# Kernel tuning notes

Hardware: AMD Instinct MI355X
Metric: run time of the kernel (lower is better)

Reference implementation:

```python
import jax, jax.numpy as jnp
import numpy as np

GROUPS = 32
EPS = 1e-6


def group_norm(x, gamma, beta):
    b, h, w, c = x.shape
    xg = x.reshape(b, h, w, GROUPS, c // GROUPS)
    mean = jnp.mean(xg, axis=(1, 2, 4), keepdims=True)
    var = jnp.var(xg, axis=(1, 2, 4), keepdims=True)
    xg = (xg - mean) * jax.lax.rsqrt(var + EPS)
    return xg.reshape(b, h, w, c) * gamma + beta


def setup_inputs() -> dict:
    key = jax.random.key(0)
    ks = jax.random.split(key, 6)
    B, H, W, C = 4, 64, 64, 512
    scale = 0.02
    return {
        "x": jax.random.normal(ks[0], (B, H, W, C), dtype=jnp.float32),
        "gamma": jnp.ones((C,), dtype=jnp.float32),
        "beta": jnp.zeros((C,), dtype=jnp.float32),
        "wq": jax.random.normal(ks[1], (C, C), dtype=jnp.float32) * scale,
        "bq": jnp.zeros((C,), dtype=jnp.float32),
        "wk": jax.random.normal(ks[2], (C, C), dtype=jnp.float32) * scale,
        "bk": jnp.zeros((C,), dtype=jnp.float32),
        "wv": jax.random.normal(ks[3], (C, C), dtype=jnp.float32) * scale,
        "bv": jnp.zeros((C,), dtype=jnp.float32),
        "wo": jax.random.normal(ks[4], (C, C), dtype=jnp.float32) * scale,
        "bo": jnp.zeros((C,), dtype=jnp.float32),
    }


def reference(x, gamma, beta, wq, bq, wk, bk, wv, bv, wo, bo):
    b, h, w, c = x.shape
    xn = group_norm(x, gamma, beta)
    # 1x1 convs == per-pixel linear layers
    q = (jnp.einsum('bhwc,cd->bhwd', xn, wq) + bq).reshape(b, h * w, c)
    k = (jnp.einsum('bhwc,cd->bhwd', xn, wk) + bk).reshape(b, h * w, c)
    v = (jnp.einsum('bhwc,cd->bhwd', xn, wv) + bv).reshape(b, h * w, c)
    # full (hw x hw) attention, single head
    scores = jnp.einsum('bic,bjc->bij', q, k) * (c ** -0.5)  # [b, hw, hw]
    attn = jax.nn.softmax(scores, axis=-1)
    out = jnp.einsum('bij,bjc->bic', attn, v).reshape(b, h, w, c)
    return jnp.einsum('bhwc,cd->bhwd', out, wo) + bo + x
```

## Files before the change

### kernel.cpp

```cpp
#include <hip/hip_runtime.h>
#include <stdint.h>


typedef __attribute__((ext_vector_type(8))) short bf16x8;
typedef __attribute__((ext_vector_type(8))) unsigned short u16x8;
typedef __attribute__((ext_vector_type(4))) float f32x4;

#define SOFTMAX_SCALE 0.044194173824159216f

__device__ __forceinline__ unsigned short f2bf(float f) {
  unsigned int x = __float_as_uint(f);
  x += 0x7fffu + ((x >> 16) & 1u);
  return (unsigned short)(x >> 16);
}
__device__ __forceinline__ float bf2f(unsigned short u) {
  return __uint_as_float((unsigned int)u << 16);
}

__device__ __forceinline__ void gl_lds16(const void* g, void* l) {
  __builtin_amdgcn_global_load_lds(
      (__attribute__((address_space(1))) unsigned char*)g,
      (__attribute__((address_space(3))) unsigned char*)l, 16, 0, 0);
}

__device__ __forceinline__ void gemm_tile(
    const unsigned short* __restrict__ A, long lda,
    const unsigned short* __restrict__ B, long ldb,
    int K, unsigned short* As, unsigned short* Bs, f32x4 acc[4][4]) {
  const int tid = threadIdx.x;
  const int wave = tid >> 6, lane = tid & 63;
  const int srow = lane >> 3;
  const int soff = ((lane & 7) ^ srow) * 16;
  const int wm = (wave >> 1) * 64, wn = (wave & 1) * 64;
  const int lrow = lane & 15;
  const int rsw = lrow & 7;
  const int kgb = lane >> 4;

  for (int k0 = 0; k0 < K; k0 += 64) {
    __syncthreads();
    for (int i = 0; i < 4; ++i) {
      int chunk = wave * 4 + i;
      int row = chunk * 8 + srow;
      gl_lds16((const char*)(A + (long)row * lda + k0) + soff, (char*)As + chunk * 1024);
      gl_lds16((const char*)(B + (long)row * ldb + k0) + soff, (char*)Bs + chunk * 1024);
    }
    __syncthreads();
#pragma unroll
    for (int ks = 0; ks < 2; ++ks) {
      bf16x8 af[4], bfr[4];
      const int off = ((ks * 4 + kgb) ^ rsw) * 8;
#pragma unroll
      for (int t = 0; t < 4; ++t) {
        af[t]  = *(const bf16x8*)&As[(wm + t * 16 + lrow) * 64 + off];
        bfr[t] = *(const bf16x8*)&Bs[(wn + t * 16 + lrow) * 64 + off];
      }
#pragma unroll
      for (int mt = 0; mt < 4; ++mt)
#pragma unroll
        for (int nt = 0; nt < 4; ++nt)
          acc[mt][nt] = __builtin_amdgcn_mfma_f32_16x16x32_bf16(af[mt], bfr[nt], acc[mt][nt], 0, 0, 0);
    }
  }
}

#define EPILOG_SETUP                                          \
  const int lane = threadIdx.x & 63, wave = threadIdx.x >> 6; \
  const int wm = (wave >> 1) * 64, wn = (wave & 1) * 64;      \
  const int lcol = lane & 15, lrb = (lane >> 4) * 4;

__global__ void prep_kernel(const float* __restrict__ wq, const float* __restrict__ wk,
                            const float* __restrict__ wv, const float* __restrict__ wo,
                            const float* __restrict__ bq, const float* __restrict__ bk,
                            const float* __restrict__ bv,
                            unsigned short* __restrict__ wqkvT,
                            unsigned short* __restrict__ woT,
                            float* __restrict__ bias, float* __restrict__ stats,
                            float* __restrict__ lsum) {
  long id = (long)blockIdx.x * 256 + threadIdx.x;
  if (id < 786432) {
    long n = id >> 9, k = id & 511;
    const float* w = (n < 512) ? wq : (n < 1024 ? wk : wv);
    wqkvT[id] = f2bf(w[k * 512 + (n & 511)]);
  } else if (id < 786432 + 262144) {
    long j = id - 786432, n = j >> 9, k = j & 511;
    woT[j] = f2bf(wo[k * 512 + n]);
  } else if (id < 786432 + 262144 + 1536) {
    long j = id - 786432 - 262144;
    bias[j] = (j < 512) ? bq[j] : (j < 1024 ? bk[j - 512] : bv[j - 1024]);
  } else if (id < 786432 + 262144 + 1536 + 256) {
    stats[id - 786432 - 262144 - 1536] = 0.f;
  } else if (id < 786432 + 262144 + 1536 + 256 + 16384) {
    lsum[id - 786432 - 262144 - 1536 - 256] = 0.f;
  }
}

__global__ __launch_bounds__(256) void gn_stats(const float* __restrict__ x,
                                                float* __restrict__ stats) {
  const int b = blockIdx.x >> 7, slab = blockIdx.x & 127;
  const float* xp = x + (long)b * 4096 * 512 + (long)slab * 32 * 512;
  const int tid = threadIdx.x;
  float s = 0.f, s2 = 0.f;
  for (int it = 0; it < 16; ++it) {
    int i = it * 256 + tid;
    float4 v = *(const float4*)(xp + (long)i * 4);
    s += v.x + v.y + v.z + v.w;
    s2 += v.x * v.x + v.y * v.y + v.z * v.z + v.w * v.w;
  }
  s += __shfl_xor(s, 1); s += __shfl_xor(s, 2);
  s2 += __shfl_xor(s2, 1); s2 += __shfl_xor(s2, 2);
  if ((tid & 3) == 0) {
    int g = (tid & 127) >> 2;
    atomicAdd(&stats[(b * 32 + g) * 2], s);
    atomicAdd(&stats[(b * 32 + g) * 2 + 1], s2);
  }
}

__global__ __launch_bounds__(256) void gn_apply(const float* __restrict__ x,
                                                const float* __restrict__ stats,
                                                const float* __restrict__ gamma,
                                                const float* __restrict__ beta,
                                                unsigned short* __restrict__ xn) {
  long id = (long)blockIdx.x * 256 + threadIdx.x;
  long a = id * 4;
  int b = (int)(id >> 19);
  int ch = (int)(a & 511);
  int g = ch >> 4;
  float s = stats[(b * 32 + g) * 2], s2 = stats[(b * 32 + g) * 2 + 1];
  float mean = s * (1.f / 65536.f);
  float rinv = rsqrtf(s2 * (1.f / 65536.f) - mean * mean + 1e-6f);
  float4 v = *(const float4*)(x + a);
  float4 gm = *(const float4*)(gamma + ch);
  float4 bt = *(const float4*)(beta + ch);
  ushort4 o;
  o.x = f2bf((v.x - mean) * rinv * gm.x + bt.x);
  o.y = f2bf((v.y - mean) * rinv * gm.y + bt.y);
  o.z = f2bf((v.z - mean) * rinv * gm.z + bt.z);
  o.w = f2bf((v.w - mean) * rinv * gm.w + bt.w);
  *(ushort4*)(xn + a) = o;
}

__global__ __launch_bounds__(256) void qkv_kernel(
    const unsigned short* __restrict__ xn, const unsigned short* __restrict__ wqkvT,
    const float* __restrict__ bias, unsigned short* __restrict__ q,
    unsigned short* __restrict__ kk, unsigned short* __restrict__ vv) {
  __shared__ unsigned short As[128 * 64], Bs[128 * 64];
  f32x4 acc[4][4] = {};
  const long tm = (long)blockIdx.x * 128, tn = (long)blockIdx.y * 128;
  gemm_tile(xn + tm * 512, 512, wqkvT + tn * 512, 512, 512, As, Bs, acc);
  EPILOG_SETUP
#pragma unroll
  for (int mt = 0; mt < 4; ++mt)
#pragma unroll
    for (int nt = 0; nt < 4; ++nt)
#pragma unroll
      for (int r = 0; r < 4; ++r) {
        long m = tm + wm + mt * 16 + lrb + r;
        long n = tn + wn + nt * 16 + lcol;
        float v = acc[mt][nt][r] + bias[n];
        if (n < 512)       q[m * 512 + n] = f2bf(v * SOFTMAX_SCALE);
        else if (n < 1024) kk[m * 512 + (n - 512)] = f2bf(v);
        else               vv[m * 512 + (n - 1024)] = f2bf(v);
      }
}

__global__ __launch_bounds__(256) void transpose_v(const unsigned short* __restrict__ v,
                                                   unsigned short* __restrict__ vT) {
  const int b = blockIdx.z;
  const long j0 = (long)blockIdx.x * 64, c0 = (long)blockIdx.y * 64;
  __shared__ unsigned short t[64][72];
  const int tc = (threadIdx.x & 15) * 4, tr = threadIdx.x >> 4;
  for (int rr = 0; rr < 64; rr += 16) {
    ushort4 u = *(const ushort4*)&v[((long)b * 4096 + j0 + tr + rr) * 512 + c0 + tc];
    t[tr + rr][tc] = u.x; t[tr + rr][tc + 1] = u.y;
    t[tr + rr][tc + 2] = u.z; t[tr + rr][tc + 3] = u.w;
  }
  __syncthreads();
  for (int rr = 0; rr < 64; rr += 16) {
    int c = tr + rr;
    ushort4 o;
    o.x = t[tc + 0][c]; o.y = t[tc + 1][c]; o.z = t[tc + 2][c]; o.w = t[tc + 3][c];
    *(ushort4*)&vT[((long)b * 512 + c0 + c) * 4096 + j0 + tc] = o;
  }
}

__global__ __launch_bounds__(256) void qkt_kernel(
    const unsigned short* __restrict__ q, const unsigned short* __restrict__ kk,
    unsigned short* __restrict__ probs, float* __restrict__ lsum, int b0) {
  __shared__ unsigned short As[128 * 64], Bs[128 * 64];
  f32x4 acc[4][4] = {};
  const int z = blockIdx.z;
  const long bb = (long)(b0 + z) * 4096 * 512;
  const long tm = (long)blockIdx.x * 128, tn = (long)blockIdx.y * 128;
  gemm_tile(q + bb + tm * 512, 512, kk + bb + tn * 512, 512, 512, As, Bs, acc);
  EPILOG_SETUP
  unsigned short* out = probs + (long)z * 4096 * 4096;
  float* ls = lsum + (long)(b0 + z) * 4096;
#pragma unroll
  for (int mt = 0; mt < 4; ++mt) {
    float rsum[4] = {0.f, 0.f, 0.f, 0.f};
#pragma unroll
    for (int nt = 0; nt < 4; ++nt)
#pragma unroll
      for (int r = 0; r < 4; ++r) {
        long m = tm + wm + mt * 16 + lrb + r;
        long n = tn + wn + nt * 16 + lcol;
        float e = __expf(acc[mt][nt][r]);
        unsigned short h = f2bf(e);
        out[m * 4096 + n] = h;
        rsum[r] += bf2f(h);
      }
#pragma unroll
    for (int r = 0; r < 4; ++r) {
      float s = rsum[r];
      s += __shfl_xor(s, 1); s += __shfl_xor(s, 2);
      s += __shfl_xor(s, 4); s += __shfl_xor(s, 8);
      if (lcol == 0) atomicAdd(&ls[tm + wm + mt * 16 + lrb + r], s);
    }
  }
}

__global__ __launch_bounds__(256) void pv_kernel(
    const unsigned short* __restrict__ probs, const unsigned short* __restrict__ vT,
    unsigned short* __restrict__ part, int b0) {
  __shared__ unsigned short As[128 * 64], Bs[128 * 64];
  f32x4 acc[4][4] = {};
  const int zb = blockIdx.z >> 2, s = blockIdx.z & 3;
  const long tm = (long)blockIdx.x * 128, tn = (long)blockIdx.y * 128;
  gemm_tile(probs + (long)zb * 4096 * 4096 + tm * 4096 + s * 1024, 4096,
            vT + (long)(b0 + zb) * 512 * 4096 + tn * 4096 + s * 1024, 4096,
            1024, As, Bs, acc);
  EPILOG_SETUP
  unsigned short* out = part + (long)blockIdx.z * 4096 * 512;
#pragma unroll
  for (int mt = 0; mt < 4; ++mt)
#pragma unroll
    for (int nt = 0; nt < 4; ++nt)
#pragma unroll
      for (int r = 0; r < 4; ++r) {
        long m = tm + wm + mt * 16 + lrb + r;
        long n = tn + wn + nt * 16 + lcol;
        out[m * 512 + n] = f2bf(acc[mt][nt][r]);
      }
}

__global__ __launch_bounds__(256) void reduce_kernel(const unsigned short* __restrict__ part,
                                                     const float* __restrict__ lsum,
                                                     unsigned short* __restrict__ attn,
                                                     int b0) {
  const long elems = 4096l * 512;
  const int zb = blockIdx.y;
  const unsigned short* pp = part + (long)zb * 4 * elems;
  long id = (long)blockIdx.x * 256 + threadIdx.x;
  long a = id * 8;
  int m = (int)(a >> 9);
  float inv = 1.f / lsum[(long)(b0 + zb) * 4096 + m];
  u16x8 p0 = *(const u16x8*)(pp + a);
  u16x8 p1 = *(const u16x8*)(pp + elems + a);
  u16x8 p2 = *(const u16x8*)(pp + 2 * elems + a);
  u16x8 p3 = *(const u16x8*)(pp + 3 * elems + a);
  u16x8 o;
#pragma unroll
  for (int j = 0; j < 8; ++j)
    o[j] = f2bf((bf2f(p0[j]) + bf2f(p1[j]) + bf2f(p2[j]) + bf2f(p3[j])) * inv);
  *(u16x8*)(attn + (long)(b0 + zb) * elems + a) = o;
}

__global__ __launch_bounds__(256) void proj_kernel(
    const unsigned short* __restrict__ attn, const unsigned short* __restrict__ woT,
    const float* __restrict__ bo, const float* __restrict__ x,
    float* __restrict__ out) {
  __shared__ unsigned short As[128 * 64], Bs[128 * 64];
  f32x4 acc[4][4] = {};
  const long tm = (long)blockIdx.x * 128, tn = (long)blockIdx.y * 128;
  gemm_tile(attn + tm * 512, 512, woT + tn * 512, 512, 512, As, Bs, acc);
  EPILOG_SETUP
#pragma unroll
  for (int mt = 0; mt < 4; ++mt)
#pragma unroll
    for (int nt = 0; nt < 4; ++nt)
#pragma unroll
      for (int r = 0; r < 4; ++r) {
        long m = tm + wm + mt * 16 + lrb + r;
        long n = tn + wn + nt * 16 + lcol;
        out[m * 512 + n] = acc[mt][nt][r] + bo[n] + x[m * 512 + n];
      }
}

extern "C" void kernel_launch(void* const* d_in, const int* in_sizes, int n_in,
                              void* d_out, int out_size, void* d_ws, size_t ws_size,
                              hipStream_t stream) {
  const float* x     = (const float*)d_in[0];
  const float* gamma = (const float*)d_in[1];
  const float* beta  = (const float*)d_in[2];
  const float* wq    = (const float*)d_in[3];
  const float* bq    = (const float*)d_in[4];
  const float* wk    = (const float*)d_in[5];
  const float* bk    = (const float*)d_in[6];
  const float* wv    = (const float*)d_in[7];
  const float* bv    = (const float*)d_in[8];
  const float* wo    = (const float*)d_in[9];
  const float* bo    = (const float*)d_in[10];

  char* p = (char*)d_ws;
  auto take = [&](size_t bytes) { char* r = p; p += (bytes + 255) & ~(size_t)255; return r; };
  const long NTOK = 16384, C = 512, HW = 4096;
  unsigned short* xn    = (unsigned short*)take(NTOK * C * 2);
  unsigned short* q     = (unsigned short*)take(NTOK * C * 2);
  unsigned short* kbuf  = (unsigned short*)take(NTOK * C * 2);
  unsigned short* vT    = (unsigned short*)take(NTOK * C * 2);
  unsigned short* wqkvT = (unsigned short*)take(1536l * 512 * 2);
  unsigned short* woT   = (unsigned short*)take(512l * 512 * 2);
  float* bias           = (float*)take(1536 * 4);
  float* stats          = (float*)take(256 * 4);
  float* lsum           = (float*)take(16384 * 4);

  size_t fixed = (size_t)(p - (char*)d_ws);
  size_t per_nb = (size_t)HW * HW * 2 + 4ul * HW * C * 2 + 512;
  int NB = (ws_size >= fixed + 4 * per_nb) ? 4
         : (ws_size >= fixed + 2 * per_nb) ? 2 : 1;
  unsigned short* probs = (unsigned short*)take((size_t)NB * HW * HW * 2);
  unsigned short* part  = (unsigned short*)take((size_t)NB * 4 * HW * C * 2);
  unsigned short* attn  = xn;
  unsigned short* vbuf  = part;

  prep_kernel<<<4168, 256, 0, stream>>>(wq, wk, wv, wo, bq, bk, bv, wqkvT, woT,
                                        bias, stats, lsum);
  gn_stats<<<512, 256, 0, stream>>>(x, stats);
  gn_apply<<<8192, 256, 0, stream>>>(x, stats, gamma, beta, xn);

  qkv_kernel<<<dim3(128, 12), 256, 0, stream>>>(xn, wqkvT, bias, q, kbuf, vbuf);
  transpose_v<<<dim3(64, 8, 4), 256, 0, stream>>>(vbuf, vT);

  for (int b0 = 0; b0 < 4; b0 += NB) {
    qkt_kernel<<<dim3(32, 32, NB), 256, 0, stream>>>(q, kbuf, probs, lsum, b0);
    pv_kernel<<<dim3(32, 4, 4 * NB), 256, 0, stream>>>(probs, vT, part, b0);
    reduce_kernel<<<dim3(1024, NB), 256, 0, stream>>>(part, lsum, attn, b0);
  }

  proj_kernel<<<dim3(128, 4), 256, 0, stream>>>(attn, woT, bo, x, (float*)d_out);
}
```

Before: 428.7 us.

## Permute B-tile columns for vectorized epilogue stores, use exp2 softmax, halve PV split-K

Changes the B-operand LDS row mapping so each lane holds four adjacent output columns. The GEMM epilogues (qkv, qkt, pv, proj) can then emit ushort4/float4 vector stores instead of scalar stores, with the B-tile swizzle adjusted to avoid bank conflicts. The Q scale now folds in log2(e) so qkt can use exp2f, and the row sum uses unrounded fp32 exponentials instead of the bf16-rounded values that are stored. PV split-K drops from 4 to 2 partitions, which halves partial-buffer traffic and reduce work but also halves grid parallelism. The V staging buffer moves into the probs region.

```diff
diff --git a/kernel.cpp b/kernel.cpp
--- a/kernel.cpp
+++ b/kernel.cpp
@@ -7,6 +7,7 @@
 typedef __attribute__((ext_vector_type(4))) float f32x4;
 
 #define SOFTMAX_SCALE 0.044194173824159216f
+#define QSCALE 0.06376237087058025f
 
 __device__ __forceinline__ unsigned short f2bf(float f) {
   unsigned int x = __float_as_uint(f);
@@ -30,7 +31,7 @@
   const int tid = threadIdx.x;
   const int wave = tid >> 6, lane = tid & 63;
   const int srow = lane >> 3;
-  const int soff = ((lane & 7) ^ srow) * 16;
+  const int gg = lane & 7;
   const int wm = (wave >> 1) * 64, wn = (wave & 1) * 64;
   const int lrow = lane & 15;
   const int rsw = lrow & 7;
@@ -41,8 +42,10 @@
     for (int i = 0; i < 4; ++i) {
       int chunk = wave * 4 + i;
       int row = chunk * 8 + srow;
-      gl_lds16((const char*)(A + (long)row * lda + k0) + soff, (char*)As + chunk * 1024);
-      gl_lds16((const char*)(B + (long)row * ldb + k0) + soff, (char*)Bs + chunk * 1024);
+      int soffA = (gg ^ srow) * 16;
+      int soffB = (gg ^ ((chunk * 2 + (srow >> 2)) & 7)) * 16;
+      gl_lds16((const char*)(A + (long)row * lda + k0) + soffA, (char*)As + chunk * 1024);
+      gl_lds16((const char*)(B + (long)row * ldb + k0) + soffB, (char*)Bs + chunk * 1024);
     }
     __syncthreads();
 #pragma unroll
@@ -52,7 +55,7 @@
 #pragma unroll
       for (int t = 0; t < 4; ++t) {
         af[t]  = *(const bf16x8*)&As[(wm + t * 16 + lrow) * 64 + off];
-        bfr[t] = *(const bf16x8*)&Bs[(wn + t * 16 + lrow) * 64 + off];
+        bfr[t] = *(const bf16x8*)&Bs[(wn + 4 * lrow + t) * 64 + off];
       }
 #pragma unroll
       for (int mt = 0; mt < 4; ++mt)
@@ -66,7 +69,7 @@
 #define EPILOG_SETUP                                          \
   const int lane = threadIdx.x & 63, wave = threadIdx.x >> 6; \
   const int wm = (wave >> 1) * 64, wn = (wave & 1) * 64;      \
-  const int lcol = lane & 15, lrb = (lane >> 4) * 4;
+  const int lcol4 = (lane & 15) * 4, lrb = (lane >> 4) * 4;
 
 __global__ void prep_kernel(const float* __restrict__ wq, const float* __restrict__ wk,
                             const float* __restrict__ wv, const float* __restrict__ wo,
@@ -148,19 +151,23 @@
   const long tm = (long)blockIdx.x * 128, tn = (long)blockIdx.y * 128;
   gemm_tile(xn + tm * 512, 512, wqkvT + tn * 512, 512, 512, As, Bs, acc);
   EPILOG_SETUP
+  const int region = (int)(tn >> 9);
+  unsigned short* dst = region == 0 ? q : (region == 1 ? kk : vv);
+  const long nloc = (tn & 511) + wn + lcol4;
+  const float sc = region == 0 ? QSCALE : 1.f;
+  float4 bs = *(const float4*)&bias[tn + wn + lcol4];
 #pragma unroll
   for (int mt = 0; mt < 4; ++mt)
 #pragma unroll
-    for (int nt = 0; nt < 4; ++nt)
-#pragma unroll
-      for (int r = 0; r < 4; ++r) {
-        long m = tm + wm + mt * 16 + lrb + r;
-        long n = tn + wn + nt * 16 + lcol;
-        float v = acc[mt][nt][r] + bias[n];
-        if (n < 512)       q[m * 512 + n] = f2bf(v * SOFTMAX_SCALE);
-        else if (n < 1024) kk[m * 512 + (n - 512)] = f2bf(v);
-        else               vv[m * 512 + (n - 1024)] = f2bf(v);
-      }
+    for (int r = 0; r < 4; ++r) {
+      long m = tm + wm + mt * 16 + lrb + r;
+      ushort4 o;
+      o.x = f2bf((acc[mt][0][r] + bs.x) * sc);
+      o.y = f2bf((acc[mt][1][r] + bs.y) * sc);
+      o.z = f2bf((acc[mt][2][r] + bs.z) * sc);
+      o.w = f2bf((acc[mt][3][r] + bs.w) * sc);
+      *(ushort4*)&dst[m * 512 + nloc] = o;
+    }
 }
 
 __global__ __launch_bounds__(256) void transpose_v(const unsigned short* __restrict__ v,
@@ -195,26 +202,28 @@
   EPILOG_SETUP
   unsigned short* out = probs + (long)z * 4096 * 4096;
   float* ls = lsum + (long)(b0 + z) * 4096;
+  const long n0 = tn + wn + lcol4;
 #pragma unroll
   for (int mt = 0; mt < 4; ++mt) {
-    float rsum[4] = {0.f, 0.f, 0.f, 0.f};
-#pragma unroll
-    for (int nt = 0; nt < 4; ++nt)
-#pragma unroll
-      for (int r = 0; r < 4; ++r) {
-        long m = tm + wm + mt * 16 + lrb + r;
-        long n = tn + wn + nt * 16 + lcol;
-        float e = __expf(acc[mt][nt][r]);
-        unsigned short h = f2bf(e);
-        out[m * 4096 + n] = h;
-        rsum[r] += bf2f(h);
-      }
-#pragma unroll
-    for (int r = 0; r < 4; ++r) {
-      float s = rsum[r];
+    float rs[4];
+#pragma unroll
+    for (int r = 0; r < 4; ++r) {
+      float e0 = exp2f(acc[mt][0][r]);
+      float e1 = exp2f(acc[mt][1][r]);
+      float e2 = exp2f(acc[mt][2][r]);
+      float e3 = exp2f(acc[mt][3][r]);
+      rs[r] = (e0 + e1) + (e2 + e3);
+      ushort4 o;
+      o.x = f2bf(e0); o.y = f2bf(e1); o.z = f2bf(e2); o.w = f2bf(e3);
+      long m = tm + wm + mt * 16 + lrb + r;
+      *(ushort4*)&out[m * 4096 + n0] = o;
+    }
+#pragma unroll
+    for (int r = 0; r < 4; ++r) {
+      float s = rs[r];
       s += __shfl_xor(s, 1); s += __shfl_xor(s, 2);
       s += __shfl_xor(s, 4); s += __shfl_xor(s, 8);
-      if (lcol == 0) atomicAdd(&ls[tm + wm + mt * 16 + lrb + r], s);
+      if (lcol4 == 0) atomicAdd(&ls[tm + wm + mt * 16 + lrb + r], s);
     }
   }
 }
@@ -224,23 +233,24 @@
     unsigned short* __restrict__ part, int b0) {
   __shared__ unsigned short As[128 * 64], Bs[128 * 64];
   f32x4 acc[4][4] = {};
-  const int zb = blockIdx.z >> 2, s = blockIdx.z & 3;
+  const int zb = blockIdx.z >> 1, s = blockIdx.z & 1;
   const long tm = (long)blockIdx.x * 128, tn = (long)blockIdx.y * 128;
-  gemm_tile(probs + (long)zb * 4096 * 4096 + tm * 4096 + s * 1024, 4096,
-            vT + (long)(b0 + zb) * 512 * 4096 + tn * 4096 + s * 1024, 4096,
-            1024, As, Bs, acc);
+  gemm_tile(probs + (long)zb * 4096 * 4096 + tm * 4096 + s * 2048, 4096,
+            vT + (long)(b0 + zb) * 512 * 4096 + tn * 4096 + s * 2048, 4096,
+            2048, As, Bs, acc);
   EPILOG_SETUP
   unsigned short* out = part + (long)blockIdx.z * 4096 * 512;
+  const long n0 = tn + wn + lcol4;
 #pragma unroll
   for (int mt = 0; mt < 4; ++mt)
 #pragma unroll
-    for (int nt = 0; nt < 4; ++nt)
-#pragma unroll
-      for (int r = 0; r < 4; ++r) {
-        long m = tm + wm + mt * 16 + lrb + r;
-        long n = tn + wn + nt * 16 + lcol;
-        out[m * 512 + n] = f2bf(acc[mt][nt][r]);
-      }
+    for (int r = 0; r < 4; ++r) {
+      long m = tm + wm + mt * 16 + lrb + r;
+      ushort4 o;
+      o.x = f2bf(acc[mt][0][r]); o.y = f2bf(acc[mt][1][r]);
+      o.z = f2bf(acc[mt][2][r]); o.w = f2bf(acc[mt][3][r]);
+      *(ushort4*)&out[m * 512 + n0] = o;
+    }
 }
 
 __global__ __launch_bounds__(256) void reduce_kernel(const unsigned short* __restrict__ part,
@@ -249,19 +259,17 @@
                                                      int b0) {
   const long elems = 4096l * 512;
   const int zb = blockIdx.y;
-  const unsigned short* pp = part + (long)zb * 4 * elems;
+  const unsigned short* pp = part + (long)zb * 2 * elems;
   long id = (long)blockIdx.x * 256 + threadIdx.x;
   long a = id * 8;
   int m = (int)(a >> 9);
   float inv = 1.f / lsum[(long)(b0 + zb) * 4096 + m];
   u16x8 p0 = *(const u16x8*)(pp + a);
   u16x8 p1 = *(const u16x8*)(pp + elems + a);
-  u16x8 p2 = *(const u16x8*)(pp + 2 * elems + a);
-  u16x8 p3 = *(const u16x8*)(pp + 3 * elems + a);
   u16x8 o;
 #pragma unroll
   for (int j = 0; j < 8; ++j)
-    o[j] = f2bf((bf2f(p0[j]) + bf2f(p1[j]) + bf2f(p2[j]) + bf2f(p3[j])) * inv);
+    o[j] = f2bf((bf2f(p0[j]) + bf2f(p1[j])) * inv);
   *(u16x8*)(attn + (long)(b0 + zb) * elems + a) = o;
 }
 
@@ -274,16 +282,21 @@
   const long tm = (long)blockIdx.x * 128, tn = (long)blockIdx.y * 128;
   gemm_tile(attn + tm * 512, 512, woT + tn * 512, 512, 512, As, Bs, acc);
   EPILOG_SETUP
+  const long n0 = tn + wn + lcol4;
+  float4 bs = *(const float4*)&bo[n0];
 #pragma unroll
   for (int mt = 0; mt < 4; ++mt)
 #pragma unroll
-    for (int nt = 0; nt < 4; ++nt)
-#pragma unroll
-      for (int r = 0; r < 4; ++r) {
-        long m = tm + wm + mt * 16 + lrb + r;
-        long n = tn + wn + nt * 16 + lcol;
-        out[m * 512 + n] = acc[mt][nt][r] + bo[n] + x[m * 512 + n];
-      }
+    for (int r = 0; r < 4; ++r) {
+      long m = tm + wm + mt * 16 + lrb + r;
+      float4 xv = *(const float4*)&x[m * 512 + n0];
+      float4 o;
+      o.x = acc[mt][0][r] + bs.x + xv.x;
+      o.y = acc[mt][1][r] + bs.y + xv.y;
+      o.z = acc[mt][2][r] + bs.z + xv.z;
+      o.w = acc[mt][3][r] + bs.w + xv.w;
+      *(float4*)&((float*)out)[m * 512 + n0] = o;
+    }
 }
 
 extern "C" void kernel_launch(void* const* d_in, const int* in_sizes, int n_in,
@@ -315,13 +328,13 @@
   float* lsum           = (float*)take(16384 * 4);
 
   size_t fixed = (size_t)(p - (char*)d_ws);
-  size_t per_nb = (size_t)HW * HW * 2 + 4ul * HW * C * 2 + 512;
+  size_t per_nb = (size_t)HW * HW * 2 + 2ul * HW * C * 2 + 512;
   int NB = (ws_size >= fixed + 4 * per_nb) ? 4
          : (ws_size >= fixed + 2 * per_nb) ? 2 : 1;
   unsigned short* probs = (unsigned short*)take((size_t)NB * HW * HW * 2);
-  unsigned short* part  = (unsigned short*)take((size_t)NB * 4 * HW * C * 2);
+  unsigned short* part  = (unsigned short*)take((size_t)NB * 2 * HW * C * 2);
   unsigned short* attn  = xn;
-  unsigned short* vbuf  = part;
+  unsigned short* vbuf  = probs;
 
   prep_kernel<<<4168, 256, 0, stream>>>(wq, wk, wv, wo, bq, bk, bv, wqkvT, woT,
                                         bias, stats, lsum);
@@ -333,7 +346,7 @@
 
   for (int b0 = 0; b0 < 4; b0 += NB) {
     qkt_kernel<<<dim3(32, 32, NB), 256, 0, stream>>>(q, kbuf, probs, lsum, b0);
-    pv_kernel<<<dim3(32, 4, 4 * NB), 256, 0, stream>>>(probs, vT, part, b0);
+    pv_kernel<<<dim3(32, 4, 2 * NB), 256, 0, stream>>>(probs, vT, part, b0);
     reduce_kernel<<<dim3(1024, NB), 256, 0, stream>>>(part, lsum, attn, b0);
   }
 
```

New measurement: 401.1 us. 6.4% less time.
